# Kernel optimization log

Measured on AMD Instinct MI355X. Metric: run time of the kernel, lower is better.

The kernel has to match this reference:

```python
import jax, jax.numpy as jnp
import numpy as np

N, E, D, L = 50000, 800000, 128, 2
EPS = 1e-10


def mobius_add(x, y, c):
    # c: shape [1], broadcasts against [N,1]
    xy = jnp.sum(x * y, axis=-1, keepdims=True)
    x2 = jnp.sum(x * x, axis=-1, keepdims=True)
    y2 = jnp.sum(y * y, axis=-1, keepdims=True)
    num = (1 + 2 * c * xy + c * y2) * x + (1 - c * x2) * y
    den = 1 + 2 * c * xy + (c ** 2) * x2 * y2
    return num / den


def log_map(x, y, c):
    ym = mobius_add(-x, y, c)
    n = jnp.maximum(jnp.linalg.norm(ym, axis=-1, keepdims=True), EPS)
    sc = jnp.sqrt(c)
    return (2.0 / sc) * jnp.arctanh(sc * n) * ym / n


def exp_map(x, v, c):
    n = jnp.maximum(jnp.linalg.norm(v, axis=-1, keepdims=True), EPS)
    sc = jnp.sqrt(c)
    second = jnp.tanh(sc * n / 2.0) * v / (sc * n)
    return mobius_add(x, second, c)


def l2norm(x):
    return x / jnp.maximum(jnp.linalg.norm(x, axis=-1, keepdims=True), 1e-12)


def mean_agg(h, src, dst, n_nodes):
    # copy_u + mean reduce: mean of h[src] grouped by dst; zero-degree -> 0
    msum = jax.ops.segment_sum(h[src], dst, num_segments=n_nodes)
    deg = jax.ops.segment_sum(jnp.ones((src.shape[0], 1), h.dtype), dst, num_segments=n_nodes)
    return msum / jnp.maximum(deg, 1.0)


def setup_inputs() -> dict:
    key = jax.random.key(0)
    ks = jax.random.split(key, 12)
    scale = 1.0 / np.sqrt(D)
    return {
        "src": jax.random.randint(ks[0], (E,), 0, N, dtype=jnp.int32),
        "dst": jax.random.randint(ks[1], (E,), 0, N, dtype=jnp.int32),
        "e_emb": jax.random.normal(ks[2], (N, D), dtype=jnp.float32),
        "b_emb": 0.01 * jax.random.normal(ks[3], (N, D), dtype=jnp.float32),  # inside Poincare ball
        "s_emb": jax.random.normal(ks[4], (N, D), dtype=jnp.float32),
        "e_W": scale * jax.random.normal(ks[5], (L, D, D), dtype=jnp.float32),
        "e_b": jnp.zeros((L, D), dtype=jnp.float32),
        "b_W": scale * jax.random.normal(ks[6], (L, D, D), dtype=jnp.float32),
        "b_b": jnp.zeros((L, D), dtype=jnp.float32),
        "s_W": scale * jax.random.normal(ks[7], (L, D, D), dtype=jnp.float32),
        "s_b": jnp.zeros((L, D), dtype=jnp.float32),
        "b_curvature": jnp.ones((1,), dtype=jnp.float32),
        "s_curvature": jnp.ones((1,), dtype=jnp.float32),
    }


def reference(src, dst, e_emb, b_emb, s_emb, e_W, e_b, b_W, b_b, s_W, s_b, b_curvature, s_curvature):
    n = e_emb.shape[0]
    origin = jnp.zeros((1, b_emb.shape[-1]), dtype=b_emb.dtype)
    for l in range(L):
        # Euclidean: transform -> mean aggregate -> LeakyReLU(0.2)
        h = e_emb @ e_W[l].T + e_b[l]
        e_emb = mean_agg(h, src, dst, n)
        e_emb = jnp.where(e_emb > 0, e_emb, 0.2 * e_emb)
        # Hyperbolic: log map to tangent -> transform -> mean aggregate -> exp map
        tangent = log_map(origin, b_emb, b_curvature)
        hb = tangent @ b_W[l].T + b_b[l]
        neigh_b = mean_agg(hb, src, dst, n)
        b_emb = exp_map(origin, neigh_b, b_curvature)
        # Spherical: normalize -> transform -> normalize -> mean aggregate -> normalize
        hs = l2norm(l2norm(s_emb) @ s_W[l].T + s_b[l])
        s_emb = l2norm(mean_agg(hs, src, dst, n))
    return (e_emb, b_emb, s_emb)
```

## Files before the change

### kernel.cpp

```cpp
#include <hip/hip_runtime.h>
#include <math.h>

#define DD 128
typedef unsigned int   u32;
typedef unsigned short u16;
typedef short bf16x8 __attribute__((ext_vector_type(8)));
typedef float f32x4  __attribute__((ext_vector_type(4)));

__device__ __forceinline__ float lo2f(u32 p){ return __uint_as_float(p << 16); }
__device__ __forceinline__ float hi2f(u32 p){ return __uint_as_float(p & 0xFFFF0000u); }
__device__ __forceinline__ u16 f2bf(float f){
    u32 u = __float_as_uint(f);
    return (u16)((u + 0x7fffu + ((u >> 16) & 1u)) >> 16);
}

__global__ void k_hist(const int* __restrict__ dst, int* __restrict__ deg, int E){
    int i = blockIdx.x*256 + threadIdx.x;
    if (i < E) atomicAdd(&deg[dst[i]], 1);
}

__global__ void k_chunksum(const int* __restrict__ deg, int* __restrict__ csum,
                           float* __restrict__ invdeg, int n){
    __shared__ int sdata[256];
    int t = threadIdx.x;
    int i0 = blockIdx.x*512 + t*2;
    int a = (i0     < n) ? deg[i0]   : 0;
    int b = (i0 + 1 < n) ? deg[i0+1] : 0;
    if (i0     < n) invdeg[i0]   = 1.0f / (float)max(a, 1);
    if (i0 + 1 < n) invdeg[i0+1] = 1.0f / (float)max(b, 1);
    sdata[t] = a + b; __syncthreads();
    for (int off = 128; off > 0; off >>= 1){
        if (t < off) sdata[t] += sdata[t+off];
        __syncthreads();
    }
    if (t == 0) csum[blockIdx.x] = sdata[0];
}

__global__ void k_scanchunks(int* __restrict__ csum, int nchunks,
                             int* __restrict__ row_ptr, int n){
    __shared__ int s[256];
    __shared__ int carry_sh;
    int t = threadIdx.x;
    if (t == 0) carry_sh = 0;
    __syncthreads();
    for (int base = 0; base < nchunks; base += 256){
        int i = base + t;
        int v = (i < nchunks) ? csum[i] : 0;
        s[t] = v;
        __syncthreads();
        for (int off = 1; off < 256; off <<= 1){
            int u = (t >= off) ? s[t-off] : 0;
            __syncthreads();
            s[t] += u;
            __syncthreads();
        }
        int carry = carry_sh;
        int excl  = carry + s[t] - v;
        if (i < nchunks) csum[i] = excl;
        int tot = s[255];
        __syncthreads();
        if (t == 0) carry_sh = carry + tot;
        __syncthreads();
    }
    if (t == 0) row_ptr[n] = carry_sh;
}

__global__ void k_scanwithin(const int* __restrict__ deg, const int* __restrict__ csum,
                             int* __restrict__ row_ptr, int* __restrict__ cursor, int n){
    __shared__ int s[256];
    int t = threadIdx.x;
    int i0 = blockIdx.x*512 + t*2;
    int a = (i0     < n) ? deg[i0]   : 0;
    int b = (i0 + 1 < n) ? deg[i0+1] : 0;
    int tsum = a + b;
    s[t] = tsum; __syncthreads();
    for (int off = 1; off < 256; off <<= 1){
        int v = (t >= off) ? s[t-off] : 0;
        __syncthreads();
        s[t] += v;
        __syncthreads();
    }
    int excl = s[t] - tsum + csum[blockIdx.x];
    if (i0     < n){ row_ptr[i0]   = excl;     cursor[i0]   = excl;     }
    if (i0 + 1 < n){ row_ptr[i0+1] = excl + a; cursor[i0+1] = excl + a; }
}

__global__ void k_fill(const int* __restrict__ src, const int* __restrict__ dst,
                       int* __restrict__ cursor, int* __restrict__ sorted_src, int E){
    int i = blockIdx.x*256 + threadIdx.x;
    if (i < E){
        int p = atomicAdd(&cursor[dst[i]], 1);
        sorted_src[p] = src[i];
    }
}

__global__ void k_w2b3(const float* __restrict__ w0, const float* __restrict__ w1,
                       const float* __restrict__ w2,
                       u16* __restrict__ o0, u16* __restrict__ o1, u16* __restrict__ o2,
                       int nw){
    int i = blockIdx.x*256 + threadIdx.x;
    if (i >= nw) return;
    const float* s = (blockIdx.y == 0) ? w0 : (blockIdx.y == 1) ? w1 : w2;
    u16*         o = (blockIdx.y == 0) ? o0 : (blockIdx.y == 1) ? o1 : o2;
    o[i] = f2bf(s[i]);
}

template<int PRE, int POST>
__device__ __forceinline__ void gemm_body(const float* __restrict__ X, const u16* __restrict__ Wb,
                                          const float* __restrict__ bias, u16* __restrict__ Y,
                                          int RS, int n_rows, const float* __restrict__ cptr){
    int t = threadIdx.x;
    int wave = t >> 6, lane = t & 63;
    int q = lane >> 4, m = lane & 15;
    int rowbase = blockIdx.x*64 + wave*16;
    int gr = min(rowbase + m, n_rows - 1);

    float4 xv[8];
    const float4* xp = (const float4*)(X + (size_t)gr*DD);
    #pragma unroll
    for (int c = 0; c < 4; c++){
        xv[2*c]   = xp[c*8 + q*2];
        xv[2*c+1] = xp[c*8 + q*2 + 1];
    }

    float scale = 1.0f;
    if (PRE != 0){
        float ss = 0.f;
        #pragma unroll
        for (int i = 0; i < 8; i++)
            ss += xv[i].x*xv[i].x + xv[i].y*xv[i].y + xv[i].z*xv[i].z + xv[i].w*xv[i].w;
        ss += __shfl_xor(ss, 16, 64);
        ss += __shfl_xor(ss, 32, 64);
        float nrm = sqrtf(ss);
        if (PRE == 1){
            float c  = cptr[0];
            c = (c > 0.f && c < 1e30f) ? c : 1.0f;
            float sc = sqrtf(c);
            float n2 = fmaxf(nrm, 1e-10f);
            float a  = fminf(sc*n2, 0.99999994f);
            scale = (2.0f/sc) * atanhf(a) / n2;
        } else {
            scale = 1.0f / fmaxf(nrm, 1e-12f);
        }
    }

    bf16x8 af[4];
    #pragma unroll
    for (int c = 0; c < 4; c++){
        const float* xf = (const float*)&xv[2*c];
        #pragma unroll
        for (int j = 0; j < 8; j++) af[c][j] = (short)f2bf(xf[j]*scale);
    }

    f32x4 acc[8];
    #pragma unroll
    for (int tl = 0; tl < 8; tl++) acc[tl] = (f32x4){0.f,0.f,0.f,0.f};

    const u16* wb = Wb + (size_t)m*DD + q*8;
    #pragma unroll
    for (int c = 0; c < 4; c++){
        #pragma unroll
        for (int tl = 0; tl < 8; tl++){
            bf16x8 bfr = *(const bf16x8*)(wb + (size_t)tl*16*DD + c*32);
            acc[tl] = __builtin_amdgcn_mfma_f32_16x16x32_bf16(af[c], bfr, acc[tl], 0, 0, 0);
        }
    }

    #pragma unroll
    for (int tl = 0; tl < 8; tl++){
        float bv = bias[tl*16 + m];
        #pragma unroll
        for (int r = 0; r < 4; r++) acc[tl][r] += bv;
    }
    if (POST == 1){
        float ssr[4] = {0.f,0.f,0.f,0.f};
        #pragma unroll
        for (int tl = 0; tl < 8; tl++)
            #pragma unroll
            for (int r = 0; r < 4; r++) ssr[r] += acc[tl][r]*acc[tl][r];
        #pragma unroll
        for (int r = 0; r < 4; r++){
            float s = ssr[r];
            s += __shfl_xor(s, 1, 64);
            s += __shfl_xor(s, 2, 64);
            s += __shfl_xor(s, 4, 64);
            s += __shfl_xor(s, 8, 64);
            float sc = 1.0f / fmaxf(sqrtf(s), 1e-12f);
            #pragma unroll
            for (int tl = 0; tl < 8; tl++) acc[tl][r] *= sc;
        }
    }
    #pragma unroll
    for (int r = 0; r < 4; r++){
        int grow = rowbase + q*4 + r;
        if (grow < n_rows){
            #pragma unroll
            for (int tl = 0; tl < 8; tl++)
                Y[(size_t)grow*RS + tl*16 + m] = f2bf(acc[tl][r]);
        }
    }
}

template<int PREB>
__global__ __launch_bounds__(256, 4)
void k_gemm3(const float* __restrict__ Xe, const float* __restrict__ Xb, const float* __restrict__ Xs,
             const u16* __restrict__ We, const u16* __restrict__ Wh, const u16* __restrict__ Ws,
             const float* __restrict__ be, const float* __restrict__ bb, const float* __restrict__ bs,
             u16* __restrict__ hEB, u16* __restrict__ hS,
             int n_rows, const float* __restrict__ cptr){
    if (blockIdx.y == 0)      gemm_body<0,0>(Xe, We, be, hEB,       256, n_rows, cptr);
    else if (blockIdx.y == 1) gemm_body<PREB,0>(Xb, Wh, bb, hEB+128, 256, n_rows, cptr);
    else                      gemm_body<2,1>(Xs, Ws, bs, hS,        128, n_rows, cptr);
}

__device__ __forceinline__ void acc8(float* a, uint4 p){
    a[0] += lo2f(p.x); a[1] += hi2f(p.x);
    a[2] += lo2f(p.y); a[3] += hi2f(p.y);
    a[4] += lo2f(p.z); a[5] += hi2f(p.z);
    a[6] += lo2f(p.w); a[7] += hi2f(p.w);
}

__global__ __launch_bounds__(256)
void k_aggT(const u32* __restrict__ hEB, const u32* __restrict__ hS,
            const int* __restrict__ row_ptr, const int* __restrict__ sorted_src,
            const float* __restrict__ invdeg,
            float* __restrict__ oE, float* __restrict__ oB, float* __restrict__ oS,
            int n_rows){
    int xcd = blockIdx.x & 7;
    int idx = blockIdx.x >> 3;

    const u32* table; int rs, coff, nodebase, hi, outcol0, path;
    {
        int hf  = xcd & 1;
        int loA = (int)(((long long)n_rows * hf) >> 1);
        int hiA = (int)(((long long)n_rows * (hf+1)) >> 1);
        int nbA = (hiA - loA + 15) >> 4;
        if (idx < nbA){
            int cA = xcd >> 1;
            table = hEB; rs = 128; coff = cA*32;
            nodebase = loA + idx*16; hi = hiA;
            path = cA >> 1; outcol0 = (cA & 1)*64;
        } else {
            int i2 = idx - nbA;
            int qd = xcd & 3;
            int loB = (int)(((long long)n_rows * qd) >> 2);
            int hiB = (int)(((long long)n_rows * (qd+1)) >> 2);
            int nbB = (hiB - loB + 15) >> 4;
            if (i2 >= nbB) return;
            int cS = xcd >> 2;
            table = hS; rs = 64; coff = cS*32;
            nodebase = loB + i2*16; hi = hiB;
            path = 2; outcol0 = cS*64;
        }
    }
    float* dest = (path == 0) ? oE : (path == 1) ? oB : oS;
    bool leaky = (path == 0);

    int w = threadIdx.x >> 6, lane = threadIdx.x & 63;
    int g = lane >> 3, l8 = lane & 7;
    const u32* tbl = table + coff + l8*4;

    for (int k = 0; k < 4; k++){
        int v = nodebase + w*4 + k;
        if (v >= hi) break;
        int beg = row_ptr[v], end = row_ptr[v+1];
        float a[8];
        #pragma unroll
        for (int i = 0; i < 8; i++) a[i] = 0.f;

        int p = beg + g;
        for (; p + 8 < end; p += 16){
            int i0 = sorted_src[p];
            int i1 = sorted_src[p+8];
            uint4 c0 = *(const uint4*)(tbl + (size_t)i0*rs);
            uint4 c1 = *(const uint4*)(tbl + (size_t)i1*rs);
            acc8(a, c0); acc8(a, c1);
        }
        if (p < end){
            int i0 = sorted_src[p];
            uint4 c0 = *(const uint4*)(tbl + (size_t)i0*rs);
            acc8(a, c0);
        }

        #pragma unroll
        for (int i = 0; i < 8; i++){
            a[i] += __shfl_xor(a[i], 8, 64);
            a[i] += __shfl_xor(a[i], 16, 64);
            a[i] += __shfl_xor(a[i], 32, 64);
        }
        if (g == 0){
            float inv = invdeg[v];
            float o[8];
            #pragma unroll
            for (int i = 0; i < 8; i++){
                float x = a[i]*inv;
                o[i] = leaky ? (x > 0.f ? x : 0.2f*x) : x;
            }
            float4* dp = (float4*)(dest + (size_t)v*DD + outcol0 + l8*8);
            dp[0] = make_float4(o[0],o[1],o[2],o[3]);
            dp[1] = make_float4(o[4],o[5],o[6],o[7]);
        }
    }
}

__global__ __launch_bounds__(256)
void k_final(const float* __restrict__ tb, const float* __restrict__ ts,
             float* __restrict__ ob, float* __restrict__ os,
             int n_rows, const float* __restrict__ cptr){
    int wid = (blockIdx.x*256 + threadIdx.x) >> 6;
    if (wid >= n_rows) return;
    int lane = threadIdx.x & 63;
    float2 vb = *(const float2*)(tb + (size_t)wid*DD + lane*2);
    float2 vs = *(const float2*)(ts + (size_t)wid*DD + lane*2);
    float ssb = vb.x*vb.x + vb.y*vb.y;
    float sss = vs.x*vs.x + vs.y*vs.y;
    #pragma unroll
    for (int m = 32; m > 0; m >>= 1){
        ssb += __shfl_xor(ssb, m, 64);
        sss += __shfl_xor(sss, m, 64);
    }
    float cc = cptr[0];
    cc = (cc > 0.f && cc < 1e30f) ? cc : 1.0f;
    float sc = sqrtf(cc);
    float nb = fmaxf(sqrtf(ssb), 1e-10f);
    float scb = tanhf(sc*nb*0.5f) / (sc*nb);
    float scs = 1.0f / fmaxf(sqrtf(sss), 1e-12f);
    *(float2*)(ob + (size_t)wid*DD + lane*2) = make_float2(vb.x*scb, vb.y*scb);
    *(float2*)(os + (size_t)wid*DD + lane*2) = make_float2(vs.x*scs, vs.y*scs);
}

extern "C" void kernel_launch(void* const* d_in, const int* in_sizes, int n_in,
                              void* d_out, int out_size, void* d_ws, size_t ws_size,
                              hipStream_t stream){
    const int*   src = (const int*)d_in[0];
    const int*   dst = (const int*)d_in[1];
    const float* emb_in[3] = {(const float*)d_in[2], (const float*)d_in[3], (const float*)d_in[4]};
    const float* W_in[3]   = {(const float*)d_in[5], (const float*)d_in[7], (const float*)d_in[9]};
    const float* b_in[3]   = {(const float*)d_in[6], (const float*)d_in[8], (const float*)d_in[10]};
    const float* b_c       = (const float*)d_in[11];

    const int E  = in_sizes[0];
    const int ND = in_sizes[2];
    const int N  = ND / DD;
    const int Lnum = in_sizes[5] / (DD*DD);
    const int nw = Lnum*DD*DD;
    const int nchunks = (N + 511) / 512;

    char* w = (char*)d_ws;
    auto alloc = [&](size_t bytes)->char*{
        char* p = w; w += (bytes + 255) & ~(size_t)255; return p;
    };
    u32*   hEB       = (u32*)  alloc((size_t)ND*4);
    u32*   hS        = (u32*)  alloc((size_t)ND*2);
    float* tb        = (float*)alloc((size_t)ND*4);
    float* ts        = (float*)alloc((size_t)ND*4);
    u16*   Wb[3];
    for (int i = 0; i < 3; i++) Wb[i] = (u16*)alloc((size_t)nw*2);
    float* invdeg    = (float*)alloc((size_t)N*4);
    int*   deg       = (int*)  alloc((size_t)N*4);
    int*   row_ptr   = (int*)  alloc((size_t)(N+1)*4);
    int*   cursor    = (int*)  alloc((size_t)N*4);
    int*   csum      = (int*)  alloc((size_t)nchunks*4);
    int*   sorted_src= (int*)  alloc((size_t)E*4);
    (void)ws_size; (void)n_in; (void)out_size;

    float* out_e = (float*)d_out;
    float* out_b = out_e + ND;
    float* out_s = out_e + 2*ND;

    hipMemsetAsync(deg, 0, (size_t)N*4, stream);

    const int TB = 256;
    k_w2b3<<<dim3((nw+TB-1)/TB, 3), TB, 0, stream>>>(W_in[0], W_in[1], W_in[2],
                                                     Wb[0], Wb[1], Wb[2], nw);
    k_hist<<<(E+TB-1)/TB, TB, 0, stream>>>(dst, deg, E);
    k_chunksum<<<nchunks, 256, 0, stream>>>(deg, csum, invdeg, N);
    k_scanchunks<<<1, 256, 0, stream>>>(csum, nchunks, row_ptr, N);
    k_scanwithin<<<nchunks, 256, 0, stream>>>(deg, csum, row_ptr, cursor, N);
    k_fill<<<(E+TB-1)/TB, TB, 0, stream>>>(src, dst, cursor, sorted_src, E);

    const int gemmblocks = (N + 63) / 64;
    const int nbA = (((N+1)/2) + 15) / 16;
    const int nbB = (((N+3)/4) + 15) / 16;
    const int aggblocks = 8 * (nbA + nbB);
    const int finblocks = (N + 3) / 4;

    const float* se = emb_in[0];
    const float* sb = emb_in[1];
    const float* ss = emb_in[2];

    for (int l = 0; l < Lnum; l++){
        bool last = (l == Lnum - 1);
        if (l == 0)
            k_gemm3<1><<<dim3(gemmblocks, 3), 256, 0, stream>>>(
                se, sb, ss,
                Wb[0] + (size_t)l*DD*DD, Wb[1] + (size_t)l*DD*DD, Wb[2] + (size_t)l*DD*DD,
                b_in[0] + (size_t)l*DD,  b_in[1] + (size_t)l*DD,  b_in[2] + (size_t)l*DD,
                (u16*)hEB, (u16*)hS, N, b_c);
        else
            k_gemm3<0><<<dim3(gemmblocks, 3), 256, 0, stream>>>(
                se, sb, ss,
                Wb[0] + (size_t)l*DD*DD, Wb[1] + (size_t)l*DD*DD, Wb[2] + (size_t)l*DD*DD,
                b_in[0] + (size_t)l*DD,  b_in[1] + (size_t)l*DD,  b_in[2] + (size_t)l*DD,
                (u16*)hEB, (u16*)hS, N, b_c);

        float* dB = last ? tb : out_b;
        float* dS = last ? ts : out_s;
        k_aggT<<<aggblocks, 256, 0, stream>>>(hEB, hS, row_ptr, sorted_src, invdeg,
                                              out_e, dB, dS, N);
        if (last)
            k_final<<<finblocks, 256, 0, stream>>>(tb, ts, out_b, out_s, N, b_c);

        se = out_e; sb = out_b; ss = out_s;
    }
}
```

Measured before the change: 567.7 us.

## Give each 8-lane group its own node in aggregation, drop cross-lane reductions

The gather-aggregate kernel now assigns one node per 8-lane group, 128 nodes per block, instead of spreading each node's edges across 8 groups of a wave. The group walks all of its node's edges serially, two at a time. This removes the shuffle reduction and the single-group write-back. Index loads and output stores become nontemporal. In exchange, high-degree nodes serialise within one group and fewer independent loads are in flight per node, which could raise latency and load imbalance.

```diff
diff --git a/kernel.cpp b/kernel.cpp
--- a/kernel.cpp
+++ b/kernel.cpp
@@ -213,6 +213,7 @@
     else                      gemm_body<2,1>(Xs, Ws, bs, hS,        128, n_rows, cptr);
 }
 
+#define NPG 4
 __device__ __forceinline__ void acc8(float* a, uint4 p){
     a[0] += lo2f(p.x); a[1] += hi2f(p.x);
     a[2] += lo2f(p.y); a[3] += hi2f(p.y);
@@ -226,80 +227,77 @@
             const float* __restrict__ invdeg,
             float* __restrict__ oE, float* __restrict__ oB, float* __restrict__ oS,
             int n_rows){
+    const int NPB = 32*NPG;
     int xcd = blockIdx.x & 7;
     int idx = blockIdx.x >> 3;
+    int nbA = (((n_rows + 1) >> 1) + NPB - 1) / NPB;
+    int nbB = (((n_rows + 3) >> 2) + NPB - 1) / NPB;
 
     const u32* table; int rs, coff, nodebase, hi, outcol0, path;
-    {
+    if (idx < nbA){
         int hf  = xcd & 1;
         int loA = (int)(((long long)n_rows * hf) >> 1);
         int hiA = (int)(((long long)n_rows * (hf+1)) >> 1);
-        int nbA = (hiA - loA + 15) >> 4;
-        if (idx < nbA){
-            int cA = xcd >> 1;
-            table = hEB; rs = 128; coff = cA*32;
-            nodebase = loA + idx*16; hi = hiA;
-            path = cA >> 1; outcol0 = (cA & 1)*64;
-        } else {
-            int i2 = idx - nbA;
-            int qd = xcd & 3;
-            int loB = (int)(((long long)n_rows * qd) >> 2);
-            int hiB = (int)(((long long)n_rows * (qd+1)) >> 2);
-            int nbB = (hiB - loB + 15) >> 4;
-            if (i2 >= nbB) return;
-            int cS = xcd >> 2;
-            table = hS; rs = 64; coff = cS*32;
-            nodebase = loB + i2*16; hi = hiB;
-            path = 2; outcol0 = cS*64;
-        }
+        int cA  = xcd >> 1;
+        table = hEB; rs = 128; coff = cA*32;
+        nodebase = loA + idx*NPB; hi = hiA;
+        path = cA >> 1; outcol0 = (cA & 1)*64;
+    } else {
+        int i2 = idx - nbA;
+        if (i2 >= nbB) return;
+        int qd  = xcd & 3;
+        int loB = (int)(((long long)n_rows * qd) >> 2);
+        int hiB = (int)(((long long)n_rows * (qd+1)) >> 2);
+        int cS  = xcd >> 2;
+        table = hS; rs = 64; coff = cS*32;
+        nodebase = loB + i2*NPB; hi = hiB;
+        path = 2; outcol0 = cS*64;
     }
     float* dest = (path == 0) ? oE : (path == 1) ? oB : oS;
     bool leaky = (path == 0);
 
-    int w = threadIdx.x >> 6, lane = threadIdx.x & 63;
-    int g = lane >> 3, l8 = lane & 7;
+    int grp = threadIdx.x >> 3;
+    int l8  = threadIdx.x & 7;
     const u32* tbl = table + coff + l8*4;
 
-    for (int k = 0; k < 4; k++){
-        int v = nodebase + w*4 + k;
-        if (v >= hi) break;
+    #pragma unroll
+    for (int k = 0; k < NPG; k++){
+        int v = nodebase + k*32 + grp;
+        if (v >= hi) continue;
         int beg = row_ptr[v], end = row_ptr[v+1];
         float a[8];
         #pragma unroll
         for (int i = 0; i < 8; i++) a[i] = 0.f;
 
-        int p = beg + g;
-        for (; p + 8 < end; p += 16){
-            int i0 = sorted_src[p];
-            int i1 = sorted_src[p+8];
+        int p = beg;
+        for (; p + 1 < end; p += 2){
+            int i0 = __builtin_nontemporal_load(sorted_src + p);
+            int i1 = __builtin_nontemporal_load(sorted_src + p + 1);
             uint4 c0 = *(const uint4*)(tbl + (size_t)i0*rs);
             uint4 c1 = *(const uint4*)(tbl + (size_t)i1*rs);
             acc8(a, c0); acc8(a, c1);
         }
         if (p < end){
-            int i0 = sorted_src[p];
+            int i0 = __builtin_nontemporal_load(sorted_src + p);
             uint4 c0 = *(const uint4*)(tbl + (size_t)i0*rs);
             acc8(a, c0);
         }
 
-        #pragma unroll
-        for (int i = 0; i < 8; i++){
-            a[i] += __shfl_xor(a[i], 8, 64);
-            a[i] += __shfl_xor(a[i], 16, 64);
-            a[i] += __shfl_xor(a[i], 32, 64);
-        }
-        if (g == 0){
-            float inv = invdeg[v];
-            float o[8];
-            #pragma unroll
-            for (int i = 0; i < 8; i++){
-                float x = a[i]*inv;
-                o[i] = leaky ? (x > 0.f ? x : 0.2f*x) : x;
-            }
-            float4* dp = (float4*)(dest + (size_t)v*DD + outcol0 + l8*8);
-            dp[0] = make_float4(o[0],o[1],o[2],o[3]);
-            dp[1] = make_float4(o[4],o[5],o[6],o[7]);
-        }
+        float inv = invdeg[v];
+        f32x4 o0, o1;
+        #pragma unroll
+        for (int i = 0; i < 4; i++){
+            float x = a[i]*inv;
+            o0[i] = (leaky && x < 0.f) ? 0.2f*x : x;
+        }
+        #pragma unroll
+        for (int i = 0; i < 4; i++){
+            float x = a[4+i]*inv;
+            o1[i] = (leaky && x < 0.f) ? 0.2f*x : x;
+        }
+        f32x4* dp = (f32x4*)(dest + (size_t)v*DD + outcol0 + l8*8);
+        __builtin_nontemporal_store(o0, dp);
+        __builtin_nontemporal_store(o1, dp+1);
     }
 }
 
@@ -380,8 +378,9 @@
     k_fill<<<(E+TB-1)/TB, TB, 0, stream>>>(src, dst, cursor, sorted_src, E);
 
     const int gemmblocks = (N + 63) / 64;
-    const int nbA = (((N+1)/2) + 15) / 16;
-    const int nbB = (((N+3)/4) + 15) / 16;
+    const int NPB = 32*NPG;
+    const int nbA = (((N+1)/2) + NPB-1) / NPB;
+    const int nbB = (((N+3)/4) + NPB-1) / NPB;
     const int aggblocks = 8 * (nbA + nbB);
     const int finblocks = (N + 3) / 4;
 
```

Result: slower. 636.0 us (+12.0%).
